# Kernel tuning notes

Hardware: AMD Instinct MI355X
Metric: run time of the kernel (lower is better)

## Reference

```python
import jax, jax.numpy as jnp
import numpy as np

N, IN_CHN, MDIM, ATT_D, NUM_CLS = 100000, 1024, 512, 128, 2
NUM_GROUP, INST_PER_GROUP = 8, 4
GROUP_SIZE = N // NUM_GROUP


def setup_inputs() -> dict:
    key = jax.random.key(0)
    ks = jax.random.split(key, 8)
    def w(k, shape, fan):
        return (jax.random.normal(k, shape, jnp.float32) / np.sqrt(fan)).astype(jnp.float32)
    return {
        "index_chunk_list": jax.random.randint(ks[0], (NUM_GROUP, GROUP_SIZE), 0, N),
        "tfeat_tensor": jax.random.normal(ks[1], (N, IN_CHN), jnp.float32),
        # DimReduction: Linear(1024 -> mDim) + ReLU (numLayer_Res = 0)
        "W1": w(ks[2], (MDIM, IN_CHN), IN_CHN), "b1": jnp.zeros((MDIM,), jnp.float32),
        # Attention: Linear(mDim -> 128), tanh, Linear(128 -> 1)
        "Wa1": w(ks[3], (ATT_D, MDIM), MDIM), "ba1": jnp.zeros((ATT_D,), jnp.float32),
        "Wa2": w(ks[4], (1, ATT_D), ATT_D), "ba2": jnp.zeros((1,), jnp.float32),
        # Classifier_1fc: Linear(mDim -> num_cls)  (dropout=0 -> identity)
        "Wc": w(ks[5], (NUM_CLS, MDIM), MDIM), "bc": jnp.zeros((NUM_CLS,), jnp.float32),
    }


def _group_forward(idx, tfeat, W1, b1, Wa1, ba1, Wa2, ba2, Wc, bc):
    # idx: [S] instance indices for one pseudo-bag
    sub = jnp.take(tfeat, idx, axis=0)                       # [S, in_chn]  gather
    mid = jax.nn.relu(sub @ W1.T + b1)                       # [S, m]       DimReduction
    a = jnp.tanh(mid @ Wa1.T + ba1) @ Wa2.T + ba2            # [S, 1]       Attention logits
    a = jax.nn.softmax(a[:, 0], axis=0)                      # [S]          softmax over instances
    att = mid * a[:, None]                                   # [S, m]       einsum('ns,n->ns')
    bag = att.sum(axis=0)                                    # [m]          attention-weighted sum
    pred = bag @ Wc.T + bc                                    # [C]          bag-level logits
    # get_cam_1d: per-instance logits from classifier weight only (no bias)
    cam = jax.nn.softmax(att @ Wc.T, axis=1)                  # [S, C]
    order = jnp.argsort(-cam[:, -1])                          # descending sort on last-class prob
    topk = jnp.concatenate([order[:INST_PER_GROUP], order[-INST_PER_GROUP:]])
    maxmin = jnp.take(mid, topk, axis=0)                      # [2k, m]  MaxMinS distill feats
    return pred, maxmin


def reference(index_chunk_list, tfeat_tensor, W1, b1, Wa1, ba1, Wa2, ba2, Wc, bc):
    f = jax.vmap(_group_forward, in_axes=(0,) + (None,) * 9)
    slide_sub_preds, slide_pseudo_feat = f(index_chunk_list, tfeat_tensor,
                                           W1, b1, Wa1, ba1, Wa2, ba2, Wc, bc)
    # [numGroup, num_cls], [numGroup, 2*instance_per_group, mDim]
    return slide_sub_preds, slide_pseudo_feat
```

## Files before the change

### kernel.cpp

```cpp
#include <hip/hip_runtime.h>
#include <stdint.h>

#define N_TOT 100000
#define IN_CHN 1024
#define MDIM 512
#define ATT_D 128
#define NUM_GROUP 8
#define GROUP_SIZE 12500
#define SEGR 98

typedef __bf16 bf16x8 __attribute__((ext_vector_type(8)));
typedef float f32x4 __attribute__((ext_vector_type(4)));
typedef unsigned short u16x8 __attribute__((ext_vector_type(8)));

__device__ __forceinline__ unsigned short f2bf(float x){
  union { float f; unsigned u; } v; v.f = x;
  unsigned r = v.u + 0x7fffu + ((v.u >> 16) & 1u);
  return (unsigned short)(r >> 16);
}
__device__ __forceinline__ float bf2f(unsigned short h){
  union { unsigned u; float f; } v; v.u = ((unsigned)h) << 16; return v.f;
}
__device__ __forceinline__ void gload16(const void* g, void* l){
  __builtin_amdgcn_global_load_lds(
      (const __attribute__((address_space(1))) unsigned int*)g,
      (__attribute__((address_space(3))) unsigned int*)l, 16, 0, 0);
}

__global__ __launch_bounds__(256) void kconv(const float* __restrict__ W1,
                                             const float* __restrict__ Wa1,
                                             unsigned short* __restrict__ W1b,
                                             unsigned short* __restrict__ Wa1b){
  int i = blockIdx.x * 256 + threadIdx.x;
  if (i < MDIM * IN_CHN) W1b[i] = f2bf(W1[i]);
  else {
    int j = i - MDIM * IN_CHN;
    if (j < ATT_D * MDIM) Wa1b[j] = f2bf(Wa1[j]);
  }
}

__global__ __launch_bounds__(256) void kgemm_mid(const int* __restrict__ idxf,
                                                 const float* __restrict__ tfeat,
                                                 const unsigned short* __restrict__ W1b,
                                                 const float* __restrict__ b1,
                                                 unsigned short* __restrict__ midb){
  __shared__ alignas(16) float A0[128 * 32];
  __shared__ alignas(16) float A1[128 * 32];
  __shared__ alignas(16) unsigned short B0[128 * 32];
  __shared__ alignas(16) unsigned short B1[128 * 32];
  __shared__ int gsm[128];
  int tid = threadIdx.x;
  int tile = (blockIdx.x & 7) * 391 + (blockIdx.x >> 3);
  int bn = tile & 3, bm = tile >> 2;
  int m0 = bm * 128, n0 = bn * 128;
  if (tid < 128){ int r = m0 + tid; gsm[tid] = idxf[r < N_TOT ? r : 0]; }
  __syncthreads();

  int w = tid >> 6, l = tid & 63;
  int l16 = tid & 15, hi = (tid >> 4) & 3;
  int wm = tid >> 7, wn = (tid >> 6) & 1;

  const float* asrc[4]; int adst[4];
  #pragma unroll
  for (int q = 0; q < 4; q++){
    int rowl = q * 32 + w * 8 + (l >> 3);
    asrc[q] = tfeat + (size_t)gsm[rowl] * IN_CHN + (((l & 7) ^ (l >> 3)) << 2);
    adst[q] = (q * 32 + w * 8) * 32;
  }
  const unsigned short* bsrc[2]; int bdst[2];
  #pragma unroll
  for (int q = 0; q < 2; q++){
    int rowl = q * 64 + w * 16 + (l >> 2);
    bsrc[q] = W1b + (size_t)(n0 + rowl) * IN_CHN + (((l & 3) ^ ((l >> 3) & 3)) << 3);
    bdst[q] = (q * 64 + w * 16) * 32;
  }

  f32x4 acc[4][4];
  #pragma unroll
  for (int a = 0; a < 4; a++)
    #pragma unroll
    for (int b = 0; b < 4; b++) acc[a][b] = (f32x4){0.f, 0.f, 0.f, 0.f};

  int r7 = l16 & 7;
  int b3 = (l16 >> 1) & 3;

  auto stage = [&](float* Ax, unsigned short* Bx, int s){
    #pragma unroll
    for (int q = 0; q < 4; q++) gload16(asrc[q] + s * 32, Ax + adst[q]);
    #pragma unroll
    for (int q = 0; q < 2; q++) gload16(bsrc[q] + s * 32, Bx + bdst[q]);
  };
  auto compute = [&](const float* Ax, const unsigned short* Bx){
    bf16x8 af[4], bfr[4];
    #pragma unroll
    for (int a = 0; a < 4; a++){
      int row = wm * 64 + a * 16 + l16;
      f32x4 lo  = *(const f32x4*)&Ax[row * 32 + (((2 * hi) ^ r7) << 2)];
      f32x4 hi4 = *(const f32x4*)&Ax[row * 32 + (((2 * hi + 1) ^ r7) << 2)];
      bf16x8 pk;
      pk[0] = (__bf16)lo[0]; pk[1] = (__bf16)lo[1]; pk[2] = (__bf16)lo[2]; pk[3] = (__bf16)lo[3];
      pk[4] = (__bf16)hi4[0]; pk[5] = (__bf16)hi4[1]; pk[6] = (__bf16)hi4[2]; pk[7] = (__bf16)hi4[3];
      af[a] = pk;
    }
    #pragma unroll
    for (int b = 0; b < 4; b++){
      int row = wn * 64 + b * 16 + l16;
      bfr[b] = *(const bf16x8*)&Bx[row * 32 + ((hi ^ b3) << 3)];
    }
    #pragma unroll
    for (int a = 0; a < 4; a++)
      #pragma unroll
      for (int b = 0; b < 4; b++)
        acc[a][b] = __builtin_amdgcn_mfma_f32_16x16x32_bf16(af[a], bfr[b], acc[a][b], 0, 0, 0);
  };

  stage(A0, B0, 0);
  __syncthreads();
  for (int s2 = 0; s2 < 32; s2 += 2){
    stage(A1, B1, s2 + 1);
    compute(A0, B0);
    __syncthreads();
    if (s2 + 2 < 32) stage(A0, B0, s2 + 2);
    compute(A1, B1);
    __syncthreads();
  }

  #pragma unroll
  for (int b = 0; b < 4; b++){
    int col = n0 + wn * 64 + b * 16 + l16;
    float bias = b1[col];
    #pragma unroll
    for (int a = 0; a < 4; a++){
      int rbase = m0 + wm * 64 + a * 16 + hi * 4;
      #pragma unroll
      for (int q = 0; q < 4; q++){
        int row = rbase + q;
        if (row < N_TOT){
          float v = acc[a][b][q] + bias;
          midb[(size_t)row * MDIM + col] = f2bf(fmaxf(v, 0.f));
        }
      }
    }
  }
}

__global__ __launch_bounds__(256) void kattn(const unsigned short* __restrict__ midb,
                                             const unsigned short* __restrict__ Wa1b,
                                             const float* __restrict__ ba1,
                                             const float* __restrict__ Wa2,
                                             const float* __restrict__ ba2,
                                             const float* __restrict__ Wc,
                                             float* __restrict__ lv,
                                             float* __restrict__ tv){
  __shared__ alignas(16) unsigned short Asm[128 * 64];
  __shared__ alignas(16) unsigned short Bsm[128 * 64];
  __shared__ float dsh[512];
  __shared__ float part[128][2];
  int tid = threadIdx.x;
  int m0 = blockIdx.x * 128;
  for (int i = tid; i < 512; i += 256) dsh[i] = Wc[512 + i] - Wc[i];

  int w = tid >> 6, l = tid & 63;
  int l16 = tid & 15, hi = (tid >> 4) & 3;
  int wm = tid >> 7, wn = (tid >> 6) & 1;
  int scw = (l & 7) ^ (l >> 3);

  const unsigned short *asrc[4], *bsrc[4];
  int dsto[4];
  #pragma unroll
  for (int q = 0; q < 4; q++){
    int rowl = q * 32 + w * 8 + (l >> 3);
    asrc[q] = midb + (size_t)(m0 + rowl) * MDIM + scw * 8;
    bsrc[q] = Wa1b + (size_t)rowl * MDIM + scw * 8;
    dsto[q] = (q * 32 + w * 8) * 64;
  }

  f32x4 acc[4][4];
  #pragma unroll
  for (int a = 0; a < 4; a++)
    #pragma unroll
    for (int b = 0; b < 4; b++) acc[a][b] = (f32x4){0.f, 0.f, 0.f, 0.f};
  int r7 = l16 & 7;

  int rt = tid >> 1, kh = tid & 1;
  int rt7 = rt & 7;
  float t = 0.f;

  for (int s = 0; s < 8; s++){
    __syncthreads();
    #pragma unroll
    for (int q = 0; q < 4; q++){
      gload16(asrc[q] + s * 64, &Asm[dsto[q]]);
      gload16(bsrc[q] + s * 64, &Bsm[dsto[q]]);
    }
    __syncthreads();
    #pragma unroll
    for (int ks = 0; ks < 2; ks++){
      bf16x8 af[4], bfr[4];
      #pragma unroll
      for (int a = 0; a < 4; a++){
        int row = wm * 64 + a * 16 + l16;
        af[a] = *(const bf16x8*)&Asm[row * 64 + (((ks * 4 + hi) ^ r7) << 3)];
      }
      #pragma unroll
      for (int b = 0; b < 4; b++){
        int row = wn * 64 + b * 16 + l16;
        bfr[b] = *(const bf16x8*)&Bsm[row * 64 + (((ks * 4 + hi) ^ r7) << 3)];
      }
      #pragma unroll
      for (int a = 0; a < 4; a++)
        #pragma unroll
        for (int b = 0; b < 4; b++)
          acc[a][b] = __builtin_amdgcn_mfma_f32_16x16x32_bf16(af[a], bfr[b], acc[a][b], 0, 0, 0);
    }
    #pragma unroll
    for (int j = 0; j < 4; j++){
      int gc = kh * 4 + j;
      u16x8 v = *(const u16x8*)&Asm[rt * 64 + ((gc ^ rt7) << 3)];
      int kb = s * 64 + gc * 8;
      #pragma unroll
      for (int e = 0; e < 8; e++) t += bf2f((unsigned short)v[e]) * dsh[kb + e];
    }
  }
  t += __shfl_xor(t, 1);
  if (kh == 0){
    int row = m0 + rt;
    if (row < N_TOT) tv[row] = t;
  }
  #pragma unroll
  for (int a = 0; a < 4; a++){
    #pragma unroll
    for (int q = 0; q < 4; q++){
      float v = 0.f;
      #pragma unroll
      for (int b = 0; b < 4; b++){
        int col = wn * 64 + b * 16 + l16;
        v += tanhf(acc[a][b][q] + ba1[col]) * Wa2[col];
      }
      #pragma unroll
      for (int off = 1; off < 16; off <<= 1) v += __shfl_xor(v, off);
      if (l16 == 0) part[wm * 64 + a * 16 + hi * 4 + q][wn] = v;
    }
  }
  __syncthreads();
  if (tid < 128){
    int row = m0 + tid;
    if (row < N_TOT) lv[row] = part[tid][0] + part[tid][1] + ba2[0];
  }
}

__global__ __launch_bounds__(256) void kselect(const float* __restrict__ lv,
                                               const float* __restrict__ tv,
                                               float* __restrict__ maxlw, float* __restrict__ Zw,
                                               int* __restrict__ cand,
                                               float* __restrict__ w){
  __shared__ float keys[GROUP_SIZE];
  __shared__ float candk[4096];
  __shared__ int   candi[4096];
  __shared__ float rk[256];
  __shared__ int ri[256];
  __shared__ int rs[256];
  __shared__ float sbc;
  int g = blockIdx.x, tid = threadIdx.x;
  const float* lg = lv + (size_t)g * GROUP_SIZE;
  const float* tg = tv + (size_t)g * GROUP_SIZE;

  float mx = -1e30f;
  for (int i = tid; i < GROUP_SIZE; i += 256) mx = fmaxf(mx, lg[i]);
  rk[tid] = mx; __syncthreads();
  for (int s = 128; s > 0; s >>= 1){ if (tid < s) rk[tid] = fmaxf(rk[tid], rk[tid + s]); __syncthreads(); }
  if (tid == 0) sbc = rk[0];
  __syncthreads();
  float maxl = sbc;

  float z = 0.f;
  for (int i = tid; i < GROUP_SIZE; i += 256){
    float ez = expf(lg[i] - maxl);
    z += ez;
    keys[i] = ez * tg[i];
  }
  rk[tid] = z; __syncthreads();
  for (int s = 128; s > 0; s >>= 1){ if (tid < s) rk[tid] += rk[tid + s]; __syncthreads(); }
  if (tid == 0){ maxlw[g] = maxl; Zw[g] = rk[0]; }
  __syncthreads();
  float invZ = 1.0f / rk[0];
  for (int i = tid; i < GROUP_SIZE; i += 256)
    w[(size_t)g * GROUP_SIZE + i] = expf(lg[i] - maxl) * invZ;
  __syncthreads();

  {
    float tk[16]; int tix[16];
    #pragma unroll
    for (int j = 0; j < 16; j++){ tk[j] = -1e30f; tix[j] = 0x7fffffff; }
    for (int i = tid; i < GROUP_SIZE; i += 256){
      float ck = keys[i];
      if (ck > tk[15]){
        int ci = i;
        #pragma unroll
        for (int j = 0; j < 16; j++){
          bool ins = ck > tk[j];
          float nk = ins ? ck : tk[j]; int ni = ins ? ci : tix[j];
          float ok = ins ? tk[j] : ck; int oi = ins ? tix[j] : ci;
          tk[j] = nk; tix[j] = ni; ck = ok; ci = oi;
        }
      }
    }
    #pragma unroll
    for (int j = 0; j < 16; j++){ candk[tid * 16 + j] = tk[j]; candi[tid * 16 + j] = tix[j]; }
  }
  __syncthreads();
  for (int it = 0; it < 16; it++){
    float bk = -1e30f; int bi = 0x7fffffff; int bs = -1;
    for (int jj = tid; jj < 4096; jj += 256){
      float k = candk[jj]; int ix = candi[jj];
      if (k > bk || (k == bk && ix < bi)){ bk = k; bi = ix; bs = jj; }
    }
    rk[tid] = bk; ri[tid] = bi; rs[tid] = bs; __syncthreads();
    for (int s = 128; s > 0; s >>= 1){
      if (tid < s){
        if (rk[tid + s] > rk[tid] || (rk[tid + s] == rk[tid] && ri[tid + s] < ri[tid])){
          rk[tid] = rk[tid + s]; ri[tid] = ri[tid + s]; rs[tid] = rs[tid + s];
        }
      }
      __syncthreads();
    }
    if (tid == 0){ cand[g * 32 + it] = ri[0]; candk[rs[0]] = -1e30f; }
    __syncthreads();
  }

  {
    float tk[16]; int tix[16];
    #pragma unroll
    for (int j = 0; j < 16; j++){ tk[j] = 1e30f; tix[j] = -1; }
    for (int i = tid; i < GROUP_SIZE; i += 256){
      float ck = keys[i];
      if (ck <= tk[15]){
        int ci = i;
        #pragma unroll
        for (int j = 0; j < 16; j++){
          bool ins = ck <= tk[j];
          float nk = ins ? ck : tk[j]; int ni = ins ? ci : tix[j];
          float ok = ins ? tk[j] : ck; int oi = ins ? tix[j] : ci;
          tk[j] = nk; tix[j] = ni; ck = ok; ci = oi;
        }
      }
    }
    #pragma unroll
    for (int j = 0; j < 16; j++){ candk[tid * 16 + j] = tk[j]; candi[tid * 16 + j] = tix[j]; }
  }
  __syncthreads();
  for (int it = 0; it < 16; it++){
    float bk = 1e30f; int bi = -1; int bs = -1;
    for (int jj = tid; jj < 4096; jj += 256){
      float k = candk[jj]; int ix = candi[jj];
      if (k < bk || (k == bk && ix > bi)){ bk = k; bi = ix; bs = jj; }
    }
    rk[tid] = bk; ri[tid] = bi; rs[tid] = bs; __syncthreads();
    for (int s = 128; s > 0; s >>= 1){
      if (tid < s){
        if (rk[tid + s] < rk[tid] || (rk[tid + s] == rk[tid] && ri[tid + s] > ri[tid])){
          rk[tid] = rk[tid + s]; ri[tid] = ri[tid + s]; rs[tid] = rs[tid + s];
        }
      }
      __syncthreads();
    }
    if (tid == 0){ cand[g * 32 + 16 + it] = ri[0]; candk[rs[0]] = 1e30f; }
    __syncthreads();
  }
}

__global__ __launch_bounds__(256) void kexact(const int* __restrict__ idxf,
                                              const float* __restrict__ tfeat,
                                              const float* __restrict__ W1,
                                              const float* __restrict__ b1,
                                              const float* __restrict__ Wa1,
                                              const float* __restrict__ ba1,
                                              const float* __restrict__ Wa2,
                                              const float* __restrict__ ba2,
                                              const float* __restrict__ Wc,
                                              const int* __restrict__ cand,
                                              const float* __restrict__ maxlw,
                                              float* __restrict__ emid, float* __restrict__ ekey){
  __shared__ float subs[1024];
  __shared__ float midc[512];
  __shared__ float hs[128];
  __shared__ float red[256];
  __shared__ float tsh;
  int bid = blockIdx.x; int g = bid >> 5, c = bid & 31; int tid = threadIdx.x;
  int s = cand[g * 32 + c];
  int inst = idxf[g * GROUP_SIZE + s];
  ((float4*)subs)[tid] = ((const float4*)(tfeat + (size_t)inst * IN_CHN))[tid];
  __syncthreads();

  float a0 = b1[tid], a1 = b1[tid + 256];
  const float4* w0 = (const float4*)(W1 + (size_t)tid * IN_CHN);
  const float4* w1 = (const float4*)(W1 + ((size_t)tid + 256) * IN_CHN);
  const float4* s4 = (const float4*)subs;
  #pragma unroll 4
  for (int k = 0; k < 256; k++){
    float4 sv = s4[k], wva = w0[k], wvb = w1[k];
    a0 += sv.x * wva.x + sv.y * wva.y + sv.z * wva.z + sv.w * wva.w;
    a1 += sv.x * wvb.x + sv.y * wvb.y + sv.z * wvb.z + sv.w * wvb.w;
  }
  a0 = fmaxf(a0, 0.f); a1 = fmaxf(a1, 0.f);
  midc[tid] = a0; midc[tid + 256] = a1;
  size_t eo = (size_t)(g * 32 + c) * MDIM;
  emid[eo + tid] = a0; emid[eo + tid + 256] = a1;
  __syncthreads();

  if (tid < 128){
    const float4* wr = (const float4*)(Wa1 + (size_t)tid * MDIM);
    const float4* m4 = (const float4*)midc;
    float h = ba1[tid];
    #pragma unroll 4
    for (int j = 0; j < 128; j++){
      float4 mv = m4[j], wv = wr[j];
      h += mv.x * wv.x + mv.y * wv.y + mv.z * wv.z + mv.w * wv.w;
    }
    hs[tid] = tanhf(h) * Wa2[tid];
  }
  __syncthreads();

  float tp = midc[tid] * (Wc[512 + tid] - Wc[tid]) + midc[tid + 256] * (Wc[768 + tid] - Wc[256 + tid]);
  red[tid] = tp; __syncthreads();
  for (int st = 128; st > 0; st >>= 1){ if (tid < st) red[tid] += red[tid + st]; __syncthreads(); }
  if (tid == 0) tsh = red[0];
  __syncthreads();
  red[tid] = (tid < 128) ? hs[tid] : 0.f; __syncthreads();
  for (int st = 128; st > 0; st >>= 1){ if (tid < st) red[tid] += red[tid + st]; __syncthreads(); }
  if (tid == 0){
    float lval = red[0] + ba2[0];
    ekey[g * 32 + c] = expf(lval - maxlw[g]) * tsh;
  }
}

__global__ __launch_bounds__(256) void kbag(const unsigned short* __restrict__ midb,
                                            const float* __restrict__ w,
                                            float* __restrict__ bagp){
  __shared__ float wl[SEGR];
  int g = blockIdx.x >> 7, seg = blockIdx.x & 127, tid = threadIdx.x;
  int i0 = seg * SEGR;
  int nr = GROUP_SIZE - i0; if (nr > SEGR) nr = SEGR;
  size_t base = (size_t)g * GROUP_SIZE;
  if (tid < nr) wl[tid] = w[base + i0 + tid];
  __syncthreads();
  float a0 = 0.f, a1 = 0.f;
  const unsigned short* mp = midb + (base + i0) * MDIM + 2 * tid;
  int i = 0;
  for (; i + 2 <= nr; i += 2){
    unsigned pk0 = *(const unsigned*)(mp + (size_t)i * MDIM);
    unsigned pk1 = *(const unsigned*)(mp + (size_t)(i + 1) * MDIM);
    float w0 = wl[i], w1 = wl[i + 1];
    a0 += w0 * bf2f((unsigned short)(pk0 & 0xffff)) + w1 * bf2f((unsigned short)(pk1 & 0xffff));
    a1 += w0 * bf2f((unsigned short)(pk0 >> 16)) + w1 * bf2f((unsigned short)(pk1 >> 16));
  }
  if (i < nr){
    unsigned pk0 = *(const unsigned*)(mp + (size_t)i * MDIM);
    float w0 = wl[i];
    a0 += w0 * bf2f((unsigned short)(pk0 & 0xffff));
    a1 += w0 * bf2f((unsigned short)(pk0 >> 16));
  }
  float* dst = bagp + (size_t)blockIdx.x * MDIM + 2 * tid;
  dst[0] = a0; dst[1] = a1;
}

__global__ __launch_bounds__(256) void kfinal(const float* __restrict__ bagp,
                                              const float* __restrict__ Wc,
                                              const float* __restrict__ bc,
                                              const float* __restrict__ emid,
                                              const float* __restrict__ ekey,
                                              const int* __restrict__ cand,
                                              float* __restrict__ out){
  __shared__ float k32[32];
  __shared__ int s32[32];
  __shared__ int ordv[32];
  __shared__ float r0[256], r1[256];
  int g = blockIdx.x, tid = threadIdx.x;
  if (tid < 32){ k32[tid] = ekey[g * 32 + tid]; s32[tid] = cand[g * 32 + tid]; }
  __syncthreads();
  if (tid == 0){
    unsigned used = 0;
    for (int a = 0; a < 32; a++){
      int best = -1;
      for (int b = 0; b < 32; b++){
        if ((used >> b) & 1u) continue;
        if (best < 0 || k32[b] > k32[best] || (k32[b] == k32[best] && s32[b] < s32[best])) best = b;
      }
      used |= 1u << best;
      ordv[a] = best;
    }
  }
  float p0 = 0.f, p1 = 0.f;
  for (int j = tid; j < 512; j += 256){
    float bv = 0.f;
    for (int s2 = 0; s2 < 128; s2++) bv += bagp[(size_t)(g * 128 + s2) * MDIM + j];
    p0 += bv * Wc[j];
    p1 += bv * Wc[512 + j];
  }
  r0[tid] = p0; r1[tid] = p1; __syncthreads();
  for (int s = 128; s > 0; s >>= 1){ if (tid < s){ r0[tid] += r0[tid + s]; r1[tid] += r1[tid + s]; } __syncthreads(); }
  if (tid == 0){
    out[g * 2 + 0] = r0[0] + bc[0];
    out[g * 2 + 1] = r1[0] + bc[1];
  }
  __syncthreads();
  for (int p = 0; p < 8; p++){
    int cc = ordv[p < 4 ? p : 24 + p];
    const float* src = emid + (size_t)(g * 32 + cc) * MDIM;
    float* dst = out + 16 + (size_t)(g * 8 + p) * MDIM;
    for (int j = tid; j < 512; j += 256) dst[j] = src[j];
  }
}

extern "C" void kernel_launch(void* const* d_in, const int* in_sizes, int n_in,
                              void* d_out, int out_size, void* d_ws, size_t ws_size,
                              hipStream_t stream){
  const int*   idxf = (const int*)d_in[0];
  const float* tfeat= (const float*)d_in[1];
  const float* W1   = (const float*)d_in[2];
  const float* b1   = (const float*)d_in[3];
  const float* Wa1  = (const float*)d_in[4];
  const float* ba1  = (const float*)d_in[5];
  const float* Wa2  = (const float*)d_in[6];
  const float* ba2  = (const float*)d_in[7];
  const float* Wc   = (const float*)d_in[8];
  const float* bc   = (const float*)d_in[9];
  float* out = (float*)d_out;
  (void)in_sizes; (void)n_in; (void)out_size; (void)ws_size;

  char* ws = (char*)d_ws;
  size_t off = 0;
  auto alloc = [&](size_t bytes){ void* p = ws + off; off += (bytes + 255) & ~(size_t)255; return p; };
  float* lv    = (float*)alloc((size_t)N_TOT * 4);
  float* tv    = (float*)alloc((size_t)N_TOT * 4);
  float* maxlw = (float*)alloc(NUM_GROUP * 4);
  float* Zw    = (float*)alloc(NUM_GROUP * 4);
  int*   cand  = (int*)alloc(NUM_GROUP * 32 * 4);
  float* ekey  = (float*)alloc(NUM_GROUP * 32 * 4);
  float* emid  = (float*)alloc((size_t)NUM_GROUP * 32 * MDIM * 4);
  float* bagp  = (float*)alloc((size_t)NUM_GROUP * 128 * MDIM * 4);
  unsigned short* W1b  = (unsigned short*)alloc((size_t)MDIM * IN_CHN * 2);
  unsigned short* Wa1b = (unsigned short*)alloc((size_t)ATT_D * MDIM * 2);
  unsigned short* midb = (unsigned short*)alloc((size_t)N_TOT * MDIM * 2);
  float* w = tv;

  kconv<<<2304, 256, 0, stream>>>(W1, Wa1, W1b, Wa1b);
  kgemm_mid<<<3128, 256, 0, stream>>>(idxf, tfeat, W1b, b1, midb);
  kattn<<<782, 256, 0, stream>>>(midb, Wa1b, ba1, Wa2, ba2, Wc, lv, tv);
  kselect<<<8, 256, 0, stream>>>(lv, tv, maxlw, Zw, cand, w);
  kexact<<<256, 256, 0, stream>>>(idxf, tfeat, W1, b1, Wa1, ba1, Wa2, ba2, Wc, cand, maxlw, emid, ekey);
  kbag<<<1024, 256, 0, stream>>>(midb, w, bagp);
  kfinal<<<8, 256, 0, stream>>>(bagp, Wc, bc, emid, ekey, cand, out);
}
```

Baseline: 669.9 us.

## Widen mid GEMM tile to 128x256 with 512 threads, single-buffered LDS

Each kgemm_mid block now covers 128 rows by 256 output columns using 8 waves, instead of 128 by 128 with 4 waves. The grid is halved and the per-XCD tile mapping is recomputed to match. Each gathered fp32 tfeat row is now fetched by 2 column tiles instead of 4, which cuts gather traffic. In exchange, the double-buffered LDS pipeline becomes a single buffer with two barriers per K step, so global loads no longer overlap with MFMA work inside a block.

New measurement: 647.0 us. 3.4% less time.

```diff
diff --git a/kernel.cpp b/kernel.cpp
--- a/kernel.cpp
+++ b/kernel.cpp
@@ -39,40 +39,39 @@
   }
 }
 
-__global__ __launch_bounds__(256) void kgemm_mid(const int* __restrict__ idxf,
+__global__ __launch_bounds__(512) void kgemm_mid(const int* __restrict__ idxf,
                                                  const float* __restrict__ tfeat,
                                                  const unsigned short* __restrict__ W1b,
                                                  const float* __restrict__ b1,
                                                  unsigned short* __restrict__ midb){
-  __shared__ alignas(16) float A0[128 * 32];
-  __shared__ alignas(16) float A1[128 * 32];
-  __shared__ alignas(16) unsigned short B0[128 * 32];
-  __shared__ alignas(16) unsigned short B1[128 * 32];
+  __shared__ alignas(16) float Af[128 * 32];
+  __shared__ alignas(16) unsigned short Bs[256 * 32];
   __shared__ int gsm[128];
   int tid = threadIdx.x;
-  int tile = (blockIdx.x & 7) * 391 + (blockIdx.x >> 3);
-  int bn = tile & 3, bm = tile >> 2;
-  int m0 = bm * 128, n0 = bn * 128;
+  int xcd = blockIdx.x & 7, idx = blockIdx.x >> 3;
+  int tile = (xcd < 4 ? xcd * 196 : 4 * 196 + (xcd - 4) * 195) + idx;
+  int bn = tile & 1, bm = tile >> 1;
+  int m0 = bm * 128, n0 = bn * 256;
   if (tid < 128){ int r = m0 + tid; gsm[tid] = idxf[r < N_TOT ? r : 0]; }
   __syncthreads();
 
   int w = tid >> 6, l = tid & 63;
   int l16 = tid & 15, hi = (tid >> 4) & 3;
-  int wm = tid >> 7, wn = (tid >> 6) & 1;
-
-  const float* asrc[4]; int adst[4];
-  #pragma unroll
-  for (int q = 0; q < 4; q++){
-    int rowl = q * 32 + w * 8 + (l >> 3);
+  int wm = w >> 2, wn = w & 3;
+
+  const float* asrc[2]; int adst[2];
+  #pragma unroll
+  for (int q = 0; q < 2; q++){
+    int rowl = q * 64 + w * 8 + (l >> 3);
     asrc[q] = tfeat + (size_t)gsm[rowl] * IN_CHN + (((l & 7) ^ (l >> 3)) << 2);
-    adst[q] = (q * 32 + w * 8) * 32;
+    adst[q] = (q * 64 + w * 8) * 32;
   }
   const unsigned short* bsrc[2]; int bdst[2];
   #pragma unroll
   for (int q = 0; q < 2; q++){
-    int rowl = q * 64 + w * 16 + (l >> 2);
+    int rowl = q * 128 + w * 16 + (l >> 2);
     bsrc[q] = W1b + (size_t)(n0 + rowl) * IN_CHN + (((l & 3) ^ ((l >> 3) & 3)) << 3);
-    bdst[q] = (q * 64 + w * 16) * 32;
+    bdst[q] = (q * 128 + w * 16) * 32;
   }
 
   f32x4 acc[4][4];
@@ -84,19 +83,21 @@
   int r7 = l16 & 7;
   int b3 = (l16 >> 1) & 3;
 
-  auto stage = [&](float* Ax, unsigned short* Bx, int s){
-    #pragma unroll
-    for (int q = 0; q < 4; q++) gload16(asrc[q] + s * 32, Ax + adst[q]);
-    #pragma unroll
-    for (int q = 0; q < 2; q++) gload16(bsrc[q] + s * 32, Bx + bdst[q]);
-  };
-  auto compute = [&](const float* Ax, const unsigned short* Bx){
+  for (int s = 0; s < 32; s++){
+    __syncthreads();
+    #pragma unroll
+    for (int q = 0; q < 2; q++){
+      gload16(asrc[q] + s * 32, &Af[adst[q]]);
+      gload16(bsrc[q] + s * 32, &Bs[bdst[q]]);
+    }
+    __syncthreads();
+
     bf16x8 af[4], bfr[4];
     #pragma unroll
     for (int a = 0; a < 4; a++){
       int row = wm * 64 + a * 16 + l16;
-      f32x4 lo  = *(const f32x4*)&Ax[row * 32 + (((2 * hi) ^ r7) << 2)];
-      f32x4 hi4 = *(const f32x4*)&Ax[row * 32 + (((2 * hi + 1) ^ r7) << 2)];
+      f32x4 lo  = *(const f32x4*)&Af[row * 32 + (((2 * hi) ^ r7) << 2)];
+      f32x4 hi4 = *(const f32x4*)&Af[row * 32 + (((2 * hi + 1) ^ r7) << 2)];
       bf16x8 pk;
       pk[0] = (__bf16)lo[0]; pk[1] = (__bf16)lo[1]; pk[2] = (__bf16)lo[2]; pk[3] = (__bf16)lo[3];
       pk[4] = (__bf16)hi4[0]; pk[5] = (__bf16)hi4[1]; pk[6] = (__bf16)hi4[2]; pk[7] = (__bf16)hi4[3];
@@ -105,24 +106,13 @@
     #pragma unroll
     for (int b = 0; b < 4; b++){
       int row = wn * 64 + b * 16 + l16;
-      bfr[b] = *(const bf16x8*)&Bx[row * 32 + ((hi ^ b3) << 3)];
+      bfr[b] = *(const bf16x8*)&Bs[row * 32 + ((hi ^ b3) << 3)];
     }
     #pragma unroll
     for (int a = 0; a < 4; a++)
       #pragma unroll
       for (int b = 0; b < 4; b++)
         acc[a][b] = __builtin_amdgcn_mfma_f32_16x16x32_bf16(af[a], bfr[b], acc[a][b], 0, 0, 0);
-  };
-
-  stage(A0, B0, 0);
-  __syncthreads();
-  for (int s2 = 0; s2 < 32; s2 += 2){
-    stage(A1, B1, s2 + 1);
-    compute(A0, B0);
-    __syncthreads();
-    if (s2 + 2 < 32) stage(A0, B0, s2 + 2);
-    compute(A1, B1);
-    __syncthreads();
   }
 
   #pragma unroll
@@ -545,7 +535,7 @@
   float* w = tv;
 
   kconv<<<2304, 256, 0, stream>>>(W1, Wa1, W1b, Wa1b);
-  kgemm_mid<<<3128, 256, 0, stream>>>(idxf, tfeat, W1b, b1, midb);
+  kgemm_mid<<<1564, 512, 0, stream>>>(idxf, tfeat, W1b, b1, midb);
   kattn<<<782, 256, 0, stream>>>(midb, Wa1b, ba1, Wa2, ba2, Wc, lv, tv);
   kselect<<<8, 256, 0, stream>>>(lv, tv, maxlw, Zw, cand, w);
   kexact<<<256, 256, 0, stream>>>(idxf, tfeat, W1, b1, Wa1, ba1, Wa2, ba2, Wc, cand, maxlw, emid, ekey);
```
